# Kernel tuning notes

Measured on AMD Instinct MI355X. Metric: run time of the kernel, lower is better.

## Reference

```python
import jax, jax.numpy as jnp
import numpy as np

N_NODES = 100000


def _graph_conv_right(feat, src, dst, W, b, n_nodes):
    # DGL GraphConv(norm='right'): since in_feats > out_feats, apply weight first,
    # then sum-aggregate messages over edges, divide by in-degree (clamped >= 1),
    # add bias, then relu activation.
    h = feat @ W                                   # [N, out]
    msg = jnp.take(h, src, axis=0)                 # [E, out] gather from source nodes
    agg = jax.ops.segment_sum(msg, dst, num_segments=n_nodes)  # [N, out]
    deg = jax.ops.segment_sum(jnp.ones_like(dst, dtype=feat.dtype), dst,
                              num_segments=n_nodes)
    deg = jnp.clip(deg, 1.0, None)                 # allow_zero_in_degree
    out = agg / deg[:, None] + b
    return jax.nn.relu(out)


def setup_inputs() -> dict:
    key = jax.random.key(0)
    ks = jax.random.split(key, 6)
    n_edges = 3200000
    in_dim, hidden_dim, out_dim = 128, 32, 12
    features = jax.random.normal(ks[0], (N_NODES, in_dim), dtype=jnp.float32)
    src = jax.random.randint(ks[1], (n_edges,), 0, N_NODES, dtype=jnp.int64 if jax.config.jax_enable_x64 else jnp.int32)
    dst = jax.random.randint(ks[2], (n_edges,), 0, N_NODES, dtype=jnp.int64 if jax.config.jax_enable_x64 else jnp.int32)
    W1 = jax.random.normal(ks[3], (in_dim, hidden_dim), dtype=jnp.float32) * (1.0 / np.sqrt(in_dim))
    b1 = jnp.zeros((hidden_dim,), dtype=jnp.float32)
    W2 = jax.random.normal(ks[4], (hidden_dim, out_dim), dtype=jnp.float32) * (1.0 / np.sqrt(hidden_dim))
    b2 = jnp.zeros((out_dim,), dtype=jnp.float32)
    return {"features": features, "src": src, "dst": dst,
            "W1": W1, "b1": b1, "W2": W2, "b2": b2}


def reference(features, src, dst, W1, b1, W2, b2):
    x = _graph_conv_right(features, src, dst, W1, b1, N_NODES)
    x = jax.nn.relu(x)  # extra F.relu after layer1 (idempotent, kept for fidelity)
    x = _graph_conv_right(x, src, dst, W2, b2, N_NODES)
    return x
```

## Files before the change

kernel.cpp:

```cpp
#include <hip/hip_runtime.h>
#include <hip/hip_fp16.h>

#define N_IN   128
#define HID    32
#define ODIM   12
#define H2P    16
#define RNODES 128
#define RSH    7
#define NBMAX  800
#define NBK    1024
#define BCAP   4608
#define CHUNK  6400

__device__ __forceinline__ void acc_f4(float (&acc)[8], float4 vf) {
    union { float4 f; __half2 h[4]; } uu; uu.f = vf;
    float2 g0 = __half22float2(uu.h[0]);
    float2 g1 = __half22float2(uu.h[1]);
    float2 g2 = __half22float2(uu.h[2]);
    float2 g3 = __half22float2(uu.h[3]);
    acc[0] += g0.x; acc[1] += g0.y;
    acc[2] += g1.x; acc[3] += g1.y;
    acc[4] += g2.x; acc[5] += g2.y;
    acc[6] += g3.x; acc[7] += g3.y;
}

__global__ __launch_bounds__(256) void gemm1_kernel(const float* __restrict__ feat,
                                                    const float* __restrict__ W1,
                                                    __half* __restrict__ h1,
                                                    int* __restrict__ bcur, int nNodes) {
    if (blockIdx.x == 0) {
        ((int4*)bcur)[threadIdx.x] = make_int4(0, 0, 0, 0);
    }
    __shared__ float sF[64 * 132];
    __shared__ float sW[N_IN * HID];
    const int tid = threadIdx.x;
    const int nb  = blockIdx.x * 64;

    {
        const float4* Wv  = (const float4*)W1;
        float4*       sWv = (float4*)sW;
        #pragma unroll
        for (int i = 0; i < 4; ++i) sWv[tid + 256 * i] = Wv[tid + 256 * i];
    }
    #pragma unroll
    for (int i = 0; i < 8; ++i) {
        int f   = tid + 256 * i;
        int row = f >> 5;
        int c4  = f & 31;
        int n   = nb + row;
        float4 v = make_float4(0.f, 0.f, 0.f, 0.f);
        if (n < nNodes) v = *(const float4*)(feat + (size_t)n * N_IN + c4 * 4);
        *(float4*)(sF + row * 132 + c4 * 4) = v;
    }
    __syncthreads();

    const int og = tid & 7;
    const int ng = tid >> 3;
    const int o0 = og * 4;
    const float* f0 = sF + ng * 132;
    const float* f1 = sF + (ng + 32) * 132;

    float acc0[4] = {0.f, 0.f, 0.f, 0.f};
    float acc1[4] = {0.f, 0.f, 0.f, 0.f};
    #pragma unroll 8
    for (int k = 0; k < N_IN; k += 4) {
        float4 a0 = *(const float4*)(f0 + k);
        float4 a1 = *(const float4*)(f1 + k);
        const float a0v[4] = {a0.x, a0.y, a0.z, a0.w};
        const float a1v[4] = {a1.x, a1.y, a1.z, a1.w};
        #pragma unroll
        for (int j = 0; j < 4; ++j) {
            float4 w = *(const float4*)(sW + (k + j) * HID + o0);
            acc0[0] += a0v[j] * w.x; acc0[1] += a0v[j] * w.y;
            acc0[2] += a0v[j] * w.z; acc0[3] += a0v[j] * w.w;
            acc1[0] += a1v[j] * w.x; acc1[1] += a1v[j] * w.y;
            acc1[2] += a1v[j] * w.z; acc1[3] += a1v[j] * w.w;
        }
    }
    int n0 = nb + ng, n1 = nb + ng + 32;
    if (n0 < nNodes) {
        union { __half2 h[2]; float2 f; } u;
        u.h[0] = __floats2half2_rn(acc0[0], acc0[1]);
        u.h[1] = __floats2half2_rn(acc0[2], acc0[3]);
        *(float2*)(h1 + (size_t)n0 * HID + o0) = u.f;
    }
    if (n1 < nNodes) {
        union { __half2 h[2]; float2 f; } u;
        u.h[0] = __floats2half2_rn(acc1[0], acc1[1]);
        u.h[1] = __floats2half2_rn(acc1[2], acc1[3]);
        *(float2*)(h1 + (size_t)n1 * HID + o0) = u.f;
    }
}

__global__ __launch_bounds__(512) void bplace_kernel(const int* __restrict__ src,
                                                     const int* __restrict__ dst,
                                                     int* __restrict__ bcur,
                                                     int* __restrict__ pairs, int nEdges) {
    __shared__ int      lh[NBK];
    __shared__ int      lcur[NBK];
    __shared__ int      gofs[NBK];
    __shared__ int      sWS[16];
    __shared__ int      lst[CHUNK];
    __shared__ unsigned short lbk[CHUNK];

    const int tid  = threadIdx.x;
    const int base = blockIdx.x * CHUNK;
    const int m    = min(CHUNK, nEdges - base);

    ((int2*)lh)[tid] = make_int2(0, 0);
    __syncthreads();

    int4 dv[3], sv[3];
    bool ok[3];
    #pragma unroll
    for (int k = 0; k < 3; ++k) {
        int e = base + k * 2048 + tid * 4;
        ok[k] = (e < nEdges);
        if (ok[k]) {
            dv[k] = *(const int4*)(dst + e);
            sv[k] = *(const int4*)(src + e);
        }
    }
    int  dt = 0, st = 0;
    bool okt = (tid < 256) && (base + 6144 + tid < nEdges);
    if (okt) {
        dt = dst[base + 6144 + tid];
        st = src[base + 6144 + tid];
    }
    #pragma unroll
    for (int k = 0; k < 3; ++k) {
        if (ok[k]) {
            atomicAdd(&lh[dv[k].x >> RSH], 1);
            atomicAdd(&lh[dv[k].y >> RSH], 1);
            atomicAdd(&lh[dv[k].z >> RSH], 1);
            atomicAdd(&lh[dv[k].w >> RSH], 1);
        }
    }
    if (okt) atomicAdd(&lh[dt >> RSH], 1);
    __syncthreads();

    int c0 = lh[2 * tid], c1 = lh[2 * tid + 1];
    int tsum = c0 + c1;
    const int lane = tid & 63, wid = tid >> 6;
    int inc = tsum;
    #pragma unroll
    for (int off = 1; off < 64; off <<= 1) {
        int t = __shfl_up(inc, off, 64);
        if (lane >= off) inc += t;
    }
    if (lane == 63) sWS[wid] = inc;
    __syncthreads();
    if (tid == 0) {
        int r = 0;
        #pragma unroll
        for (int w = 0; w < 8; ++w) { int s = sWS[w]; sWS[8 + w] = r; r += s; }
    }
    __syncthreads();
    int excl = sWS[8 + wid] + inc - tsum;
    lh[2 * tid]       = excl;
    lh[2 * tid + 1]   = excl + c0;
    lcur[2 * tid]     = excl;
    lcur[2 * tid + 1] = excl + c0;
    gofs[2 * tid]     = (c0 > 0) ? atomicAdd(&bcur[2 * tid], c0) : 0;
    gofs[2 * tid + 1] = (c1 > 0) ? atomicAdd(&bcur[2 * tid + 1], c1) : 0;
    __syncthreads();

    #pragma unroll
    for (int k = 0; k < 3; ++k) {
        if (ok[k]) {
            int b, p;
            b = dv[k].x >> RSH; p = atomicAdd(&lcur[b], 1); lst[p] = ((dv[k].x & (RNODES - 1)) << 17) | sv[k].x; lbk[p] = (unsigned short)b;
            b = dv[k].y >> RSH; p = atomicAdd(&lcur[b], 1); lst[p] = ((dv[k].y & (RNODES - 1)) << 17) | sv[k].y; lbk[p] = (unsigned short)b;
            b = dv[k].z >> RSH; p = atomicAdd(&lcur[b], 1); lst[p] = ((dv[k].z & (RNODES - 1)) << 17) | sv[k].z; lbk[p] = (unsigned short)b;
            b = dv[k].w >> RSH; p = atomicAdd(&lcur[b], 1); lst[p] = ((dv[k].w & (RNODES - 1)) << 17) | sv[k].w; lbk[p] = (unsigned short)b;
        }
    }
    if (okt) {
        int b = dt >> RSH, p = atomicAdd(&lcur[b], 1);
        lst[p] = ((dt & (RNODES - 1)) << 17) | st; lbk[p] = (unsigned short)b;
    }
    __syncthreads();

    for (int i = tid; i < m; i += 512) {
        int b = lbk[i];
        int rank = gofs[b] + (i - lh[b]);
        if (rank < BCAP) pairs[(size_t)b * BCAP + rank] = lst[i];
    }
}

__global__ __launch_bounds__(512) void sort_kernel(const int* __restrict__ bcur,
                                                   int* __restrict__ pairs,
                                                   int* __restrict__ rowstartg,
                                                   int* __restrict__ countg, int nNodes) {
    __shared__ int sorted[BCAP];
    __shared__ int hist[RNODES];
    __shared__ int scn[RNODES];
    __shared__ int cur[RNODES];
    __shared__ int sws[2];
    const int tid = threadIdx.x;
    const int bkt = blockIdx.x;
    const int cnt = min(bcur[bkt], BCAP);
    const size_t pb = (size_t)bkt * BCAP;

    if (tid < RNODES) hist[tid] = 0;
    __syncthreads();

    int vreg[9];
    #pragma unroll
    for (int u = 0; u < 9; ++u) {
        int i = tid + u * 512;
        if (i < cnt) {
            int v = pairs[pb + i];
            vreg[u] = v;
            atomicAdd(&hist[v >> 17], 1);
        }
    }
    __syncthreads();

    int v0 = 0, inc = 0;
    if (tid < RNODES) {
        v0 = hist[tid];
        inc = v0;
        #pragma unroll
        for (int off = 1; off < 64; off <<= 1) {
            int t = __shfl_up(inc, off, 64);
            if ((tid & 63) >= off) inc += t;
        }
        if ((tid & 63) == 63) sws[tid >> 6] = inc;
    }
    __syncthreads();
    if (tid < RNODES) {
        int add = (tid >= 64) ? sws[0] : 0;
        scn[tid] = add + inc - v0;
        cur[tid] = add + inc - v0;
    }
    __syncthreads();

    #pragma unroll
    for (int u = 0; u < 9; ++u) {
        int i = tid + u * 512;
        if (i < cnt) {
            int v = vreg[u];
            int pos = atomicAdd(&cur[v >> 17], 1);
            sorted[pos] = v & 0x1FFFF;
        }
    }
    __syncthreads();

    for (int i = tid; i < cnt; i += 512) pairs[pb + i] = sorted[i];
    if (tid < RNODES) {
        int n = bkt * RNODES + tid;
        if (n < nNodes) {
            rowstartg[n] = (int)pb + scn[tid];
            countg[n]    = hist[tid];
        }
    }
}

__global__ __launch_bounds__(256) void gather1_kernel(const __half* __restrict__ h1,
                                                      const int* __restrict__ rowstartg,
                                                      const int* __restrict__ countg,
                                                      const int* __restrict__ eidx,
                                                      const float* __restrict__ b1,
                                                      const float* __restrict__ W2,
                                                      __half* __restrict__ h2, int nNodes) {
    __shared__ float sW2[HID * ODIM];
    const int tid = threadIdx.x;
    if (tid < 96) ((float4*)sW2)[tid] = ((const float4*)W2)[tid];
    __syncthreads();

    const int r   = tid & 7;
    const int grp = tid >> 3;
    const int q   = r & 3;
    const int sub = r >> 2;
    const int n   = blockIdx.x * 32 + grp;
    if (n >= nNodes) return;

    const float4* h1q = (const float4*)h1;
    const int dcnt = countg[n];
    const int beg  = rowstartg[n];
    const int end  = beg + dcnt;

    float acc[8] = {0.f, 0.f, 0.f, 0.f, 0.f, 0.f, 0.f, 0.f};
    int i = beg;
    for (; i + 16 <= end; i += 16) {
        float4 v[8];
        #pragma unroll
        for (int u = 0; u < 8; ++u) {
            int e = eidx[i + 2 * u + sub];
            v[u] = h1q[(size_t)e * 4 + q];
        }
        #pragma unroll
        for (int u = 0; u < 8; ++u) acc_f4(acc, v[u]);
    }
    for (; i + 2 <= end; i += 2) {
        int e = eidx[i + sub];
        acc_f4(acc, h1q[(size_t)e * 4 + q]);
    }
    if (i < end && sub == 0) {
        int e = eidx[i];
        acc_f4(acc, h1q[(size_t)e * 4 + q]);
    }

    #pragma unroll
    for (int t = 0; t < 8; ++t) acc[t] += __shfl_xor(acc[t], 4, 8);

    const float rd = 1.f / (float)(dcnt < 1 ? 1 : dcnt);
    float x[8];
    #pragma unroll
    for (int t = 0; t < 8; ++t) {
        float xv = acc[t] * rd + b1[8 * q + t];
        x[t] = xv > 0.f ? xv : 0.f;
    }

    const int j0  = r;
    const int j1m = (r < 4) ? (r + 8) : r;
    float o0 = 0.f, o1 = 0.f;
    #pragma unroll
    for (int qq = 0; qq < 4; ++qq) {
        #pragma unroll
        for (int t = 0; t < 8; ++t) {
            float xv = __shfl(x[t], qq, 8);
            int k = 8 * qq + t;
            o0 += xv * sW2[k * ODIM + j0];
            o1 += xv * sW2[k * ODIM + j1m];
        }
    }
    h2[(size_t)n * H2P + j0] = __float2half(o0);
    if (r < 4) h2[(size_t)n * H2P + 8 + r] = __float2half(o1);
}

__global__ __launch_bounds__(256) void agg2_kernel(const __half* __restrict__ h2,
                                                   const int* __restrict__ rowstartg,
                                                   const int* __restrict__ countg,
                                                   const int* __restrict__ eidx,
                                                   const float* __restrict__ b2,
                                                   float* __restrict__ out, int nNodes) {
    const int tid = threadIdx.x;
    const int grp = tid >> 3;
    const int r   = tid & 7;
    const int n   = blockIdx.x * 32 + grp;
    if (n >= nNodes) return;

    const int half = r & 1;
    const int sub  = r >> 1;
    const float4* h2q = (const float4*)h2;

    const int cnt = countg[n];
    const int beg = rowstartg[n];
    const int end = beg + cnt;

    float acc[8] = {0.f, 0.f, 0.f, 0.f, 0.f, 0.f, 0.f, 0.f};
    int i = beg;
    for (; i + 32 <= end; i += 32) {
        float4 v[8];
        #pragma unroll
        for (int u = 0; u < 8; ++u) {
            int e = eidx[i + 4 * u + sub];
            v[u] = h2q[(size_t)e * 2 + half];
        }
        #pragma unroll
        for (int u = 0; u < 8; ++u) acc_f4(acc, v[u]);
    }
    for (; i + 4 <= end; i += 4) {
        int e = eidx[i + sub];
        acc_f4(acc, h2q[(size_t)e * 2 + half]);
    }
    const int rem = end - i;
    if (sub < rem) {
        int e = eidx[i + sub];
        acc_f4(acc, h2q[(size_t)e * 2 + half]);
    }

    #pragma unroll
    for (int t = 0; t < 8; ++t) {
        acc[t] += __shfl_xor(acc[t], 2, 8);
        acc[t] += __shfl_xor(acc[t], 4, 8);
    }

    const float rd = 1.f / (float)(cnt < 1 ? 1 : cnt);
    if (r == 0) {
        float w[8];
        #pragma unroll
        for (int t = 0; t < 8; ++t) {
            float wv = acc[t] * rd + b2[t];
            w[t] = wv > 0.f ? wv : 0.f;
        }
        *(float4*)(out + (size_t)n * ODIM)     = make_float4(w[0], w[1], w[2], w[3]);
        *(float4*)(out + (size_t)n * ODIM + 4) = make_float4(w[4], w[5], w[6], w[7]);
    } else if (r == 1) {
        float w[4];
        #pragma unroll
        for (int t = 0; t < 4; ++t) {
            float wv = acc[t] * rd + b2[8 + t];
            w[t] = wv > 0.f ? wv : 0.f;
        }
        *(float4*)(out + (size_t)n * ODIM + 8) = make_float4(w[0], w[1], w[2], w[3]);
    }
}

extern "C" void kernel_launch(void* const* d_in, const int* in_sizes, int n_in,
                              void* d_out, int out_size, void* d_ws, size_t ws_size,
                              hipStream_t stream) {
    const float* feat = (const float*)d_in[0];
    const int*   src  = (const int*)d_in[1];
    const int*   dst  = (const int*)d_in[2];
    const float* W1   = (const float*)d_in[3];
    const float* b1   = (const float*)d_in[4];
    const float* W2   = (const float*)d_in[5];
    const float* b2   = (const float*)d_in[6];
    float* out = (float*)d_out;

    const int nEdges = in_sizes[1];
    const int nNodes = in_sizes[0] / N_IN;
    const int nb     = (nNodes + RNODES - 1) / RNODES;

    __half* h1       = (__half*)d_ws;
    __half* h2       = h1 + (size_t)nNodes * HID;
    int*    rowstart = (int*)(h2 + (size_t)nNodes * H2P);
    int*    countg   = rowstart + nNodes;
    int*    bcur     = countg + nNodes;
    int*    pairs    = bcur + NBK;

    gemm1_kernel<<<(nNodes + 63) / 64, 256, 0, stream>>>(feat, W1, h1, bcur, nNodes);
    bplace_kernel<<<(nEdges + CHUNK - 1) / CHUNK, 512, 0, stream>>>(src, dst, bcur, pairs, nEdges);
    sort_kernel<<<nb, 512, 0, stream>>>(bcur, pairs, rowstart, countg, nNodes);
    gather1_kernel<<<(nNodes + 31) / 32, 256, 0, stream>>>(h1, rowstart, countg, pairs, b1, W2, h2, nNodes);
    agg2_kernel<<<(nNodes + 31) / 32, 256, 0, stream>>>(h2, rowstart, countg, pairs, b2, out, nNodes);
}
```

Before: 225.7 us.

## Fuse GEMM1 with bucket placement and sort buckets in shared memory per layer

The first GEMM and the edge bucket-placement work are merged into one heterogeneous launch, with every fourth block doing placement, so the compute-bound and scatter-bound phases overlap. The separate global sort pass and the rowstart/count arrays are removed. Each aggregation kernel now re-sorts its half-bucket (64 nodes) in shared memory and reads neighbor indices from LDS. This saves a global write and read of the sorted edge list and one launch, but each half-block reads the whole bucket, so the pairs array is read twice per layer. A small zero kernel is added to reset the bucket counters.

```diff
diff --git a/kernel.cpp b/kernel.cpp
--- a/kernel.cpp
+++ b/kernel.cpp
@@ -10,7 +10,8 @@
 #define NBMAX  800
 #define NBK    1024
 #define BCAP   4608
-#define CHUNK  6400
+#define HCAP   2560
+#define CHUNK3 3200
 
 __device__ __forceinline__ void acc_f4(float (&acc)[8], float4 vf) {
     union { float4 f; __half2 h[4]; } uu; uu.f = vf;
@@ -24,185 +25,186 @@
     acc[6] += g3.x; acc[7] += g3.y;
 }
 
-__global__ __launch_bounds__(256) void gemm1_kernel(const float* __restrict__ feat,
-                                                    const float* __restrict__ W1,
-                                                    __half* __restrict__ h1,
-                                                    int* __restrict__ bcur, int nNodes) {
-    if (blockIdx.x == 0) {
-        ((int4*)bcur)[threadIdx.x] = make_int4(0, 0, 0, 0);
-    }
-    __shared__ float sF[64 * 132];
-    __shared__ float sW[N_IN * HID];
-    const int tid = threadIdx.x;
-    const int nb  = blockIdx.x * 64;
-
-    {
-        const float4* Wv  = (const float4*)W1;
-        float4*       sWv = (float4*)sW;
-        #pragma unroll
-        for (int i = 0; i < 4; ++i) sWv[tid + 256 * i] = Wv[tid + 256 * i];
-    }
-    #pragma unroll
-    for (int i = 0; i < 8; ++i) {
-        int f   = tid + 256 * i;
-        int row = f >> 5;
-        int c4  = f & 31;
-        int n   = nb + row;
-        float4 v = make_float4(0.f, 0.f, 0.f, 0.f);
-        if (n < nNodes) v = *(const float4*)(feat + (size_t)n * N_IN + c4 * 4);
-        *(float4*)(sF + row * 132 + c4 * 4) = v;
-    }
-    __syncthreads();
-
-    const int og = tid & 7;
-    const int ng = tid >> 3;
-    const int o0 = og * 4;
-    const float* f0 = sF + ng * 132;
-    const float* f1 = sF + (ng + 32) * 132;
-
-    float acc0[4] = {0.f, 0.f, 0.f, 0.f};
-    float acc1[4] = {0.f, 0.f, 0.f, 0.f};
-    #pragma unroll 8
-    for (int k = 0; k < N_IN; k += 4) {
-        float4 a0 = *(const float4*)(f0 + k);
-        float4 a1 = *(const float4*)(f1 + k);
-        const float a0v[4] = {a0.x, a0.y, a0.z, a0.w};
-        const float a1v[4] = {a1.x, a1.y, a1.z, a1.w};
-        #pragma unroll
-        for (int j = 0; j < 4; ++j) {
-            float4 w = *(const float4*)(sW + (k + j) * HID + o0);
-            acc0[0] += a0v[j] * w.x; acc0[1] += a0v[j] * w.y;
-            acc0[2] += a0v[j] * w.z; acc0[3] += a0v[j] * w.w;
-            acc1[0] += a1v[j] * w.x; acc1[1] += a1v[j] * w.y;
-            acc1[2] += a1v[j] * w.z; acc1[3] += a1v[j] * w.w;
-        }
-    }
-    int n0 = nb + ng, n1 = nb + ng + 32;
-    if (n0 < nNodes) {
-        union { __half2 h[2]; float2 f; } u;
-        u.h[0] = __floats2half2_rn(acc0[0], acc0[1]);
-        u.h[1] = __floats2half2_rn(acc0[2], acc0[3]);
-        *(float2*)(h1 + (size_t)n0 * HID + o0) = u.f;
-    }
-    if (n1 < nNodes) {
-        union { __half2 h[2]; float2 f; } u;
-        u.h[0] = __floats2half2_rn(acc1[0], acc1[1]);
-        u.h[1] = __floats2half2_rn(acc1[2], acc1[3]);
-        *(float2*)(h1 + (size_t)n1 * HID + o0) = u.f;
-    }
-}
-
-__global__ __launch_bounds__(512) void bplace_kernel(const int* __restrict__ src,
+__global__ __launch_bounds__(256) void zero_kernel(int* __restrict__ bcur) {
+    ((int4*)bcur)[threadIdx.x] = make_int4(0, 0, 0, 0);
+}
+
+__global__ __launch_bounds__(256) void fusedA_kernel(const float* __restrict__ feat,
+                                                     const float* __restrict__ W1,
+                                                     __half* __restrict__ h1,
+                                                     const int* __restrict__ src,
                                                      const int* __restrict__ dst,
                                                      int* __restrict__ bcur,
-                                                     int* __restrict__ pairs, int nEdges) {
-    __shared__ int      lh[NBK];
-    __shared__ int      lcur[NBK];
-    __shared__ int      gofs[NBK];
-    __shared__ int      sWS[16];
-    __shared__ int      lst[CHUNK];
-    __shared__ unsigned short lbk[CHUNK];
-
-    const int tid  = threadIdx.x;
-    const int base = blockIdx.x * CHUNK;
-    const int m    = min(CHUNK, nEdges - base);
-
-    ((int2*)lh)[tid] = make_int2(0, 0);
-    __syncthreads();
-
-    int4 dv[3], sv[3];
-    bool ok[3];
-    #pragma unroll
-    for (int k = 0; k < 3; ++k) {
-        int e = base + k * 2048 + tid * 4;
-        ok[k] = (e < nEdges);
-        if (ok[k]) {
-            dv[k] = *(const int4*)(dst + e);
-            sv[k] = *(const int4*)(src + e);
-        }
-    }
-    int  dt = 0, st = 0;
-    bool okt = (tid < 256) && (base + 6144 + tid < nEdges);
-    if (okt) {
-        dt = dst[base + 6144 + tid];
-        st = src[base + 6144 + tid];
-    }
-    #pragma unroll
-    for (int k = 0; k < 3; ++k) {
-        if (ok[k]) {
-            atomicAdd(&lh[dv[k].x >> RSH], 1);
-            atomicAdd(&lh[dv[k].y >> RSH], 1);
-            atomicAdd(&lh[dv[k].z >> RSH], 1);
-            atomicAdd(&lh[dv[k].w >> RSH], 1);
-        }
-    }
-    if (okt) atomicAdd(&lh[dt >> RSH], 1);
-    __syncthreads();
-
-    int c0 = lh[2 * tid], c1 = lh[2 * tid + 1];
-    int tsum = c0 + c1;
-    const int lane = tid & 63, wid = tid >> 6;
-    int inc = tsum;
-    #pragma unroll
-    for (int off = 1; off < 64; off <<= 1) {
-        int t = __shfl_up(inc, off, 64);
-        if (lane >= off) inc += t;
-    }
-    if (lane == 63) sWS[wid] = inc;
-    __syncthreads();
-    if (tid == 0) {
-        int r = 0;
-        #pragma unroll
-        for (int w = 0; w < 8; ++w) { int s = sWS[w]; sWS[8 + w] = r; r += s; }
-    }
-    __syncthreads();
-    int excl = sWS[8 + wid] + inc - tsum;
-    lh[2 * tid]       = excl;
-    lh[2 * tid + 1]   = excl + c0;
-    lcur[2 * tid]     = excl;
-    lcur[2 * tid + 1] = excl + c0;
-    gofs[2 * tid]     = (c0 > 0) ? atomicAdd(&bcur[2 * tid], c0) : 0;
-    gofs[2 * tid + 1] = (c1 > 0) ? atomicAdd(&bcur[2 * tid + 1], c1) : 0;
-    __syncthreads();
-
-    #pragma unroll
-    for (int k = 0; k < 3; ++k) {
-        if (ok[k]) {
-            int b, p;
-            b = dv[k].x >> RSH; p = atomicAdd(&lcur[b], 1); lst[p] = ((dv[k].x & (RNODES - 1)) << 17) | sv[k].x; lbk[p] = (unsigned short)b;
-            b = dv[k].y >> RSH; p = atomicAdd(&lcur[b], 1); lst[p] = ((dv[k].y & (RNODES - 1)) << 17) | sv[k].y; lbk[p] = (unsigned short)b;
-            b = dv[k].z >> RSH; p = atomicAdd(&lcur[b], 1); lst[p] = ((dv[k].z & (RNODES - 1)) << 17) | sv[k].z; lbk[p] = (unsigned short)b;
-            b = dv[k].w >> RSH; p = atomicAdd(&lcur[b], 1); lst[p] = ((dv[k].w & (RNODES - 1)) << 17) | sv[k].w; lbk[p] = (unsigned short)b;
-        }
-    }
-    if (okt) {
-        int b = dt >> RSH, p = atomicAdd(&lcur[b], 1);
-        lst[p] = ((dt & (RNODES - 1)) << 17) | st; lbk[p] = (unsigned short)b;
-    }
-    __syncthreads();
-
-    for (int i = tid; i < m; i += 512) {
-        int b = lbk[i];
-        int rank = gofs[b] + (i - lh[b]);
-        if (rank < BCAP) pairs[(size_t)b * BCAP + rank] = lst[i];
-    }
-}
-
-__global__ __launch_bounds__(512) void sort_kernel(const int* __restrict__ bcur,
-                                                   int* __restrict__ pairs,
-                                                   int* __restrict__ rowstartg,
-                                                   int* __restrict__ countg, int nNodes) {
-    __shared__ int sorted[BCAP];
-    __shared__ int hist[RNODES];
-    __shared__ int scn[RNODES];
-    __shared__ int cur[RNODES];
-    __shared__ int sws[2];
+                                                     int* __restrict__ pairs,
+                                                     int nNodes, int nEdges, int bpGrid) {
+    union Smem {
+        struct { float sF[32 * 132]; float sW[N_IN * HID]; } g;
+        struct { int lh[NBK]; int lcur[NBK]; int gofs[NBK]; int sWS[8];
+                 int lst[CHUNK3]; unsigned short lbk[CHUNK3]; } b;
+    };
+    __shared__ Smem sm;
     const int tid = threadIdx.x;
-    const int bkt = blockIdx.x;
+    const int bid = blockIdx.x;
+    const int bq  = bid >> 2;
+
+    if ((bid & 3) == 3 && bq < bpGrid) {
+        int* lh   = sm.b.lh;
+        int* lcur = sm.b.lcur;
+        int* gofs = sm.b.gofs;
+        int* sWS  = sm.b.sWS;
+        int* lst  = sm.b.lst;
+        unsigned short* lbk = sm.b.lbk;
+
+        const int base = bq * CHUNK3;
+        const int m    = min(CHUNK3, nEdges - base);
+
+        ((int4*)lh)[tid] = make_int4(0, 0, 0, 0);
+        __syncthreads();
+
+        int4 dv[3], sv[3];
+        bool ok[3];
+        #pragma unroll
+        for (int k = 0; k < 3; ++k) {
+            int e = base + k * 1024 + tid * 4;
+            ok[k] = (e < nEdges);
+            if (ok[k]) {
+                dv[k] = *(const int4*)(dst + e);
+                sv[k] = *(const int4*)(src + e);
+            }
+        }
+        int  dt = 0, st = 0;
+        bool okt = (tid < 128) && (base + 3072 + tid < nEdges);
+        if (okt) { dt = dst[base + 3072 + tid]; st = src[base + 3072 + tid]; }
+
+        #pragma unroll
+        for (int k = 0; k < 3; ++k) {
+            if (ok[k]) {
+                atomicAdd(&lh[dv[k].x >> RSH], 1);
+                atomicAdd(&lh[dv[k].y >> RSH], 1);
+                atomicAdd(&lh[dv[k].z >> RSH], 1);
+                atomicAdd(&lh[dv[k].w >> RSH], 1);
+            }
+        }
+        if (okt) atomicAdd(&lh[dt >> RSH], 1);
+        __syncthreads();
+
+        int4 c = ((int4*)lh)[tid];
+        int tsum = c.x + c.y + c.z + c.w;
+        const int lane = tid & 63, wid = tid >> 6;
+        int inc = tsum;
+        #pragma unroll
+        for (int off = 1; off < 64; off <<= 1) {
+            int t = __shfl_up(inc, off, 64);
+            if (lane >= off) inc += t;
+        }
+        if (lane == 63) sWS[wid] = inc;
+        __syncthreads();
+        if (tid == 0) {
+            int r = 0;
+            #pragma unroll
+            for (int w = 0; w < 4; ++w) { int s = sWS[w]; sWS[4 + w] = r; r += s; }
+        }
+        __syncthreads();
+        int excl = sWS[4 + wid] + inc - tsum;
+        const int b0 = 4 * tid;
+        int e0 = excl, e1 = e0 + c.x, e2 = e1 + c.y, e3 = e2 + c.z;
+        lh[b0]   = e0; lh[b0+1]   = e1; lh[b0+2]   = e2; lh[b0+3]   = e3;
+        lcur[b0] = e0; lcur[b0+1] = e1; lcur[b0+2] = e2; lcur[b0+3] = e3;
+        gofs[b0]   = (c.x > 0) ? atomicAdd(&bcur[b0],   c.x) : 0;
+        gofs[b0+1] = (c.y > 0) ? atomicAdd(&bcur[b0+1], c.y) : 0;
+        gofs[b0+2] = (c.z > 0) ? atomicAdd(&bcur[b0+2], c.z) : 0;
+        gofs[b0+3] = (c.w > 0) ? atomicAdd(&bcur[b0+3], c.w) : 0;
+        __syncthreads();
+
+        #pragma unroll
+        for (int k = 0; k < 3; ++k) {
+            if (ok[k]) {
+                int b, p;
+                b = dv[k].x >> RSH; p = atomicAdd(&lcur[b], 1); lst[p] = ((dv[k].x & (RNODES-1)) << 17) | sv[k].x; lbk[p] = (unsigned short)b;
+                b = dv[k].y >> RSH; p = atomicAdd(&lcur[b], 1); lst[p] = ((dv[k].y & (RNODES-1)) << 17) | sv[k].y; lbk[p] = (unsigned short)b;
+                b = dv[k].z >> RSH; p = atomicAdd(&lcur[b], 1); lst[p] = ((dv[k].z & (RNODES-1)) << 17) | sv[k].z; lbk[p] = (unsigned short)b;
+                b = dv[k].w >> RSH; p = atomicAdd(&lcur[b], 1); lst[p] = ((dv[k].w & (RNODES-1)) << 17) | sv[k].w; lbk[p] = (unsigned short)b;
+            }
+        }
+        if (okt) {
+            int b = dt >> RSH, p = atomicAdd(&lcur[b], 1);
+            lst[p] = ((dt & (RNODES-1)) << 17) | st; lbk[p] = (unsigned short)b;
+        }
+        __syncthreads();
+
+        for (int i = tid; i < m; i += 256) {
+            int b = lbk[i];
+            int rank = gofs[b] + (i - lh[b]);
+            if (rank < BCAP) pairs[(size_t)b * BCAP + rank] = lst[i];
+        }
+    } else {
+        const int gb = bid - min((bid + 1) >> 2, bpGrid);
+        const int nb = gb * 32;
+
+        {
+            const float4* Wv  = (const float4*)W1;
+            float4*       sWv = (float4*)sm.g.sW;
+            #pragma unroll
+            for (int i = 0; i < 4; ++i) sWv[tid + 256 * i] = Wv[tid + 256 * i];
+        }
+        #pragma unroll
+        for (int i = 0; i < 4; ++i) {
+            int f   = tid + 256 * i;
+            int row = f >> 5;
+            int c4  = f & 31;
+            int n   = nb + row;
+            float4 v = make_float4(0.f, 0.f, 0.f, 0.f);
+            if (n < nNodes) v = *(const float4*)(feat + (size_t)n * N_IN + c4 * 4);
+            *(float4*)(sm.g.sF + row * 132 + c4 * 4) = v;
+        }
+        __syncthreads();
+
+        const int og = tid & 7;
+        const int ng = tid >> 3;
+        const int o0 = og * 4;
+        const float* f0 = sm.g.sF + ng * 132;
+
+        float acc0[4] = {0.f, 0.f, 0.f, 0.f};
+        #pragma unroll 8
+        for (int k = 0; k < N_IN; k += 4) {
+            float4 a0 = *(const float4*)(f0 + k);
+            const float a0v[4] = {a0.x, a0.y, a0.z, a0.w};
+            #pragma unroll
+            for (int j = 0; j < 4; ++j) {
+                float4 w = *(const float4*)(sm.g.sW + (k + j) * HID + o0);
+                acc0[0] += a0v[j] * w.x; acc0[1] += a0v[j] * w.y;
+                acc0[2] += a0v[j] * w.z; acc0[3] += a0v[j] * w.w;
+            }
+        }
+        int n0 = nb + ng;
+        if (n0 < nNodes) {
+            union { __half2 h[2]; float2 f; } u;
+            u.h[0] = __floats2half2_rn(acc0[0], acc0[1]);
+            u.h[1] = __floats2half2_rn(acc0[2], acc0[3]);
+            *(float2*)(h1 + (size_t)n0 * HID + o0) = u.f;
+        }
+    }
+}
+
+__global__ __launch_bounds__(512) void l1_kernel(const __half* __restrict__ h1,
+                                                 const int* __restrict__ bcur,
+                                                 const int* __restrict__ pairs,
+                                                 const float* __restrict__ b1,
+                                                 const float* __restrict__ W2,
+                                                 __half* __restrict__ h2, int nNodes) {
+    __shared__ int   sorted[HCAP];
+    __shared__ int   hist[64];
+    __shared__ int   scn[64];
+    __shared__ int   cur[64];
+    __shared__ float sW2[HID * ODIM];
+    const int tid = threadIdx.x;
+    const int bkt = blockIdx.x >> 1;
+    const int h   = blockIdx.x & 1;
     const int cnt = min(bcur[bkt], BCAP);
     const size_t pb = (size_t)bkt * BCAP;
 
-    if (tid < RNODES) hist[tid] = 0;
+    if (tid < 64) hist[tid] = 0;
+    if (tid < 96) ((float4*)sW2)[tid] = ((const float4*)W2)[tid];
     __syncthreads();
 
     int vreg[9];
@@ -212,27 +214,20 @@
         if (i < cnt) {
             int v = pairs[pb + i];
             vreg[u] = v;
-            atomicAdd(&hist[v >> 17], 1);
-        }
-    }
-    __syncthreads();
-
-    int v0 = 0, inc = 0;
-    if (tid < RNODES) {
-        v0 = hist[tid];
-        inc = v0;
+            if (((v >> 17) >> 6) == h) atomicAdd(&hist[(v >> 17) & 63], 1);
+        }
+    }
+    __syncthreads();
+
+    if (tid < 64) {
+        int v0 = hist[tid], inc = v0;
         #pragma unroll
         for (int off = 1; off < 64; off <<= 1) {
             int t = __shfl_up(inc, off, 64);
-            if ((tid & 63) >= off) inc += t;
-        }
-        if ((tid & 63) == 63) sws[tid >> 6] = inc;
-    }
-    __syncthreads();
-    if (tid < RNODES) {
-        int add = (tid >= 64) ? sws[0] : 0;
-        scn[tid] = add + inc - v0;
-        cur[tid] = add + inc - v0;
+            if (tid >= off) inc += t;
+        }
+        scn[tid] = inc - v0;
+        cur[tid] = inc - v0;
     }
     __syncthreads();
 
@@ -241,44 +236,24 @@
         int i = tid + u * 512;
         if (i < cnt) {
             int v = vreg[u];
-            int pos = atomicAdd(&cur[v >> 17], 1);
-            sorted[pos] = v & 0x1FFFF;
-        }
-    }
-    __syncthreads();
-
-    for (int i = tid; i < cnt; i += 512) pairs[pb + i] = sorted[i];
-    if (tid < RNODES) {
-        int n = bkt * RNODES + tid;
-        if (n < nNodes) {
-            rowstartg[n] = (int)pb + scn[tid];
-            countg[n]    = hist[tid];
-        }
-    }
-}
-
-__global__ __launch_bounds__(256) void gather1_kernel(const __half* __restrict__ h1,
-                                                      const int* __restrict__ rowstartg,
-                                                      const int* __restrict__ countg,
-                                                      const int* __restrict__ eidx,
-                                                      const float* __restrict__ b1,
-                                                      const float* __restrict__ W2,
-                                                      __half* __restrict__ h2, int nNodes) {
-    __shared__ float sW2[HID * ODIM];
-    const int tid = threadIdx.x;
-    if (tid < 96) ((float4*)sW2)[tid] = ((const float4*)W2)[tid];
+            if (((v >> 17) >> 6) == h) {
+                int pos = atomicAdd(&cur[(v >> 17) & 63], 1);
+                if (pos < HCAP) sorted[pos] = v & 0x1FFFF;
+            }
+        }
+    }
     __syncthreads();
 
     const int r   = tid & 7;
     const int grp = tid >> 3;
     const int q   = r & 3;
     const int sub = r >> 2;
-    const int n   = blockIdx.x * 32 + grp;
+    const int n   = bkt * RNODES + h * 64 + grp;
     if (n >= nNodes) return;
 
     const float4* h1q = (const float4*)h1;
-    const int dcnt = countg[n];
-    const int beg  = rowstartg[n];
+    const int dcnt = hist[grp];
+    const int beg  = scn[grp];
     const int end  = beg + dcnt;
 
     float acc[8] = {0.f, 0.f, 0.f, 0.f, 0.f, 0.f, 0.f, 0.f};
@@ -287,18 +262,18 @@
         float4 v[8];
         #pragma unroll
         for (int u = 0; u < 8; ++u) {
-            int e = eidx[i + 2 * u + sub];
+            int e = sorted[i + 2 * u + sub];
             v[u] = h1q[(size_t)e * 4 + q];
         }
         #pragma unroll
         for (int u = 0; u < 8; ++u) acc_f4(acc, v[u]);
     }
     for (; i + 2 <= end; i += 2) {
-        int e = eidx[i + sub];
+        int e = sorted[i + sub];
         acc_f4(acc, h1q[(size_t)e * 4 + q]);
     }
     if (i < end && sub == 0) {
-        int e = eidx[i];
+        int e = sorted[i];
         acc_f4(acc, h1q[(size_t)e * 4 + q]);
     }
 
@@ -330,25 +305,72 @@
     if (r < 4) h2[(size_t)n * H2P + 8 + r] = __float2half(o1);
 }
 
-__global__ __launch_bounds__(256) void agg2_kernel(const __half* __restrict__ h2,
-                                                   const int* __restrict__ rowstartg,
-                                                   const int* __restrict__ countg,
-                                                   const int* __restrict__ eidx,
-                                                   const float* __restrict__ b2,
-                                                   float* __restrict__ out, int nNodes) {
+__global__ __launch_bounds__(512) void l2_kernel(const __half* __restrict__ h2,
+                                                 const int* __restrict__ bcur,
+                                                 const int* __restrict__ pairs,
+                                                 const float* __restrict__ b2,
+                                                 float* __restrict__ out, int nNodes) {
+    __shared__ int sorted[HCAP];
+    __shared__ int hist[64];
+    __shared__ int scn[64];
+    __shared__ int cur[64];
     const int tid = threadIdx.x;
-    const int grp = tid >> 3;
-    const int r   = tid & 7;
-    const int n   = blockIdx.x * 32 + grp;
-    if (n >= nNodes) return;
-
+    const int bkt = blockIdx.x >> 1;
+    const int h   = blockIdx.x & 1;
+    const int cnt = min(bcur[bkt], BCAP);
+    const size_t pb = (size_t)bkt * BCAP;
+
+    if (tid < 64) hist[tid] = 0;
+    __syncthreads();
+
+    int vreg[9];
+    #pragma unroll
+    for (int u = 0; u < 9; ++u) {
+        int i = tid + u * 512;
+        if (i < cnt) {
+            int v = pairs[pb + i];
+            vreg[u] = v;
+            if (((v >> 17) >> 6) == h) atomicAdd(&hist[(v >> 17) & 63], 1);
+        }
+    }
+    __syncthreads();
+
+    if (tid < 64) {
+        int v0 = hist[tid], inc = v0;
+        #pragma unroll
+        for (int off = 1; off < 64; off <<= 1) {
+            int t = __shfl_up(inc, off, 64);
+            if (tid >= off) inc += t;
+        }
+        scn[tid] = inc - v0;
+        cur[tid] = inc - v0;
+    }
+    __syncthreads();
+
+    #pragma unroll
+    for (int u = 0; u < 9; ++u) {
+        int i = tid + u * 512;
+        if (i < cnt) {
+            int v = vreg[u];
+            if (((v >> 17) >> 6) == h) {
+                int pos = atomicAdd(&cur[(v >> 17) & 63], 1);
+                if (pos < HCAP) sorted[pos] = v & 0x1FFFF;
+            }
+        }
+    }
+    __syncthreads();
+
+    const int r    = tid & 7;
+    const int grp  = tid >> 3;
     const int half = r & 1;
     const int sub  = r >> 1;
+    const int n    = bkt * RNODES + h * 64 + grp;
+    if (n >= nNodes) return;
+
     const float4* h2q = (const float4*)h2;
-
-    const int cnt = countg[n];
-    const int beg = rowstartg[n];
-    const int end = beg + cnt;
+    const int dcnt = hist[grp];
+    const int beg  = scn[grp];
+    const int end  = beg + dcnt;
 
     float acc[8] = {0.f, 0.f, 0.f, 0.f, 0.f, 0.f, 0.f, 0.f};
     int i = beg;
@@ -356,19 +378,19 @@
         float4 v[8];
         #pragma unroll
         for (int u = 0; u < 8; ++u) {
-            int e = eidx[i + 4 * u + sub];
+            int e = sorted[i + 4 * u + sub];
             v[u] = h2q[(size_t)e * 2 + half];
         }
         #pragma unroll
         for (int u = 0; u < 8; ++u) acc_f4(acc, v[u]);
     }
     for (; i + 4 <= end; i += 4) {
-        int e = eidx[i + sub];
+        int e = sorted[i + sub];
         acc_f4(acc, h2q[(size_t)e * 2 + half]);
     }
     const int rem = end - i;
     if (sub < rem) {
-        int e = eidx[i + sub];
+        int e = sorted[i + sub];
         acc_f4(acc, h2q[(size_t)e * 2 + half]);
     }
 
@@ -378,7 +400,7 @@
         acc[t] += __shfl_xor(acc[t], 4, 8);
     }
 
-    const float rd = 1.f / (float)(cnt < 1 ? 1 : cnt);
+    const float rd = 1.f / (float)(dcnt < 1 ? 1 : dcnt);
     if (r == 0) {
         float w[8];
         #pragma unroll
@@ -413,18 +435,18 @@
 
     const int nEdges = in_sizes[1];
     const int nNodes = in_sizes[0] / N_IN;
-    const int nb     = (nNodes + RNODES - 1) / RNODES;
-
-    __half* h1       = (__half*)d_ws;
-    __half* h2       = h1 + (size_t)nNodes * HID;
-    int*    rowstart = (int*)(h2 + (size_t)nNodes * H2P);
-    int*    countg   = rowstart + nNodes;
-    int*    bcur     = countg + nNodes;
-    int*    pairs    = bcur + NBK;
-
-    gemm1_kernel<<<(nNodes + 63) / 64, 256, 0, stream>>>(feat, W1, h1, bcur, nNodes);
-    bplace_kernel<<<(nEdges + CHUNK - 1) / CHUNK, 512, 0, stream>>>(src, dst, bcur, pairs, nEdges);
-    sort_kernel<<<nb, 512, 0, stream>>>(bcur, pairs, rowstart, countg, nNodes);
-    gather1_kernel<<<(nNodes + 31) / 32, 256, 0, stream>>>(h1, rowstart, countg, pairs, b1, W2, h2, nNodes);
-    agg2_kernel<<<(nNodes + 31) / 32, 256, 0, stream>>>(h2, rowstart, countg, pairs, b2, out, nNodes);
-}
+    const int gpGrid = (nNodes + 31) / 32;
+    const int bpGrid = (nEdges + CHUNK3 - 1) / CHUNK3;
+    const int hbGrid = (nNodes + 63) / 64;
+
+    __half* h1    = (__half*)d_ws;
+    __half* h2    = h1 + (size_t)nNodes * HID;
+    int*    bcur  = (int*)(h2 + (size_t)nNodes * H2P);
+    int*    pairs = bcur + NBK;
+
+    zero_kernel<<<1, 256, 0, stream>>>(bcur);
+    fusedA_kernel<<<gpGrid + bpGrid, 256, 0, stream>>>(feat, W1, h1, src, dst, bcur,
+                                                       pairs, nNodes, nEdges, bpGrid);
+    l1_kernel<<<hbGrid, 512, 0, stream>>>(h1, bcur, pairs, b1, W2, h2, nNodes);
+    l2_kernel<<<hbGrid, 512, 0, stream>>>(h2, bcur, pairs, b2, out, nNodes);
+}
```

Result: slower. 286.5 us (+26.9%).
